# Performance work log

Measured on AMD Instinct MI355X. Metric: run time of the kernel, lower is better.

Reference implementation:

```python
import jax, jax.numpy as jnp
import numpy as np

B, H, S, D = 2, 16, 2048, 64  # depth = dmodel / num_heads
DMODEL = H * D


def setup_inputs() -> dict:
    key = jax.random.key(0)
    kq, kk, kv, kw = jax.random.split(key, 4)
    Q = jax.random.normal(kq, (B, H, S, D), dtype=jnp.float32)
    K = jax.random.normal(kk, (B, H, S, D), dtype=jnp.float32)
    V = jax.random.normal(kv, (B, H, S, D), dtype=jnp.float32)
    W = jax.random.normal(kw, (DMODEL, DMODEL), dtype=jnp.float32) * (1.0 / np.sqrt(DMODEL))
    b = jnp.zeros((DMODEL,), dtype=jnp.float32)
    return {"Q": Q, "K": K, "V": V, "W": W, "b": b}


def reference(Q, K, V, W, b):
    depth = Q.shape[-1]
    # scores: (B, H, S, S) -- full score matrix, matching the original math
    scores = jnp.einsum('bhqd,bhkd->bhqk', Q, K) / jnp.sqrt(jnp.float32(depth))
    attn = jax.nn.softmax(scores, axis=-1)
    vals = jnp.einsum('bhqk,bhkd->bhqd', attn, V)          # (B, H, S, D)
    vals = jnp.transpose(vals, (0, 2, 1, 3))               # (B, S, H, D)
    concat = vals.reshape(vals.shape[0], vals.shape[1], -1)  # (B, S, dmodel)
    return concat @ W + b
```

## Files before the change

### kernel.cpp

```cpp
#include <hip/hip_runtime.h>
#include <hip/hip_bf16.h>


typedef float  f32x16 __attribute__((ext_vector_type(16)));
typedef float  f32x4v __attribute__((ext_vector_type(4)));
typedef float  f32x2v __attribute__((ext_vector_type(2)));
typedef __bf16 bf16x8 __attribute__((ext_vector_type(8)));
typedef __bf16 bf16x4 __attribute__((ext_vector_type(4)));
typedef __bf16 bf16x2 __attribute__((ext_vector_type(2)));

static constexpr int Bn = 2, Hn = 16, Sn = 2048, Dn = 64, DM = 1024;
static constexpr size_t QKV_ELEMS = (size_t)Bn * Hn * Sn * Dn;

#define QSCALE 0.18033688011112042f

#define LGKM_BARRIER() do {                                  \
    asm volatile("s_waitcnt lgkmcnt(0)" ::: "memory");       \
    __builtin_amdgcn_s_barrier();                            \
  } while (0)

#if __has_builtin(__builtin_amdgcn_cvt_pk_bf16_f32)
static __device__ __forceinline__ unsigned pack2(float a, float b) {
  bf16x2 t = __builtin_amdgcn_cvt_pk_bf16_f32(a, b);
  union { bf16x2 v; unsigned u; } c; c.v = t; return c.u;
}
#else
static __device__ __forceinline__ unsigned pack2(float a, float b) {
  union { __bf16 h; unsigned short s; } ua, ub;
  ua.h = (__bf16)a; ub.h = (__bf16)b;
  return (unsigned)ua.s | ((unsigned)ub.s << 16);
}
#endif

static __device__ __forceinline__ void unzip8(const unsigned* wds, bf16x8* r0, bf16x8* r1) {
  union { unsigned u[4]; bf16x8 v; } a, b;
#pragma unroll
  for (int i = 0; i < 4; ++i) {
    unsigned lo = wds[2 * i], hi = wds[2 * i + 1];
    a.u[i] = (lo & 0xffffu) | (hi << 16);
    b.u[i] = (lo >> 16) | (hi & 0xffff0000u);
  }
  *r0 = a.v; *r1 = b.v;
}

__global__ __launch_bounds__(256) void convert_all(
    const float* __restrict__ k,
    const float* __restrict__ v, const float* __restrict__ w,
    __bf16* __restrict__ ko,
    __bf16* __restrict__ vt, __bf16* __restrict__ wt) {
  __shared__ __bf16 T[64][74];
  const int bid = blockIdx.x, t = threadIdx.x;

  if (bid < 2048) {
    size_t i = ((size_t)bid * 256 + t) * 8;
    f32x4v a = *(const f32x4v*)(k + i);
    f32x4v b = *(const f32x4v*)(k + i + 4);
    bf16x8 o;
#pragma unroll
    for (int j = 0; j < 4; ++j) { o[j] = (__bf16)a[j]; o[4 + j] = (__bf16)b[j]; }
    *(bf16x8*)(ko + i) = o;
    return;
  }

  const float* s0;
  __bf16* dst0;
  size_t dst_stride;
  {
    const int r = t >> 2, c0 = (t & 3) * 16;
    if (bid < 3072) {
      const int idx = bid - 2048;
      const int kv0 = (idx & 31) * 64, bh = idx >> 5;
      s0 = v + ((size_t)bh * Sn + kv0 + r) * Dn + c0;
      dst0 = vt + (size_t)bh * Dn * Sn + kv0;
      dst_stride = Sn;
    } else {
      const int idx = bid - 3072;
      const int nt = (idx & 15) * 64, kt = (idx >> 4) * 64;
      s0 = w + (size_t)(kt + r) * DM + nt + c0;
      dst0 = wt + (size_t)nt * DM + kt;
      dst_stride = DM;
    }
    union { bf16x8 v8; unsigned u[4]; } o0, o1;
#pragma unroll
    for (int i = 0; i < 2; ++i) {
      f32x4v f = *(const f32x4v*)(s0 + i * 4);
#pragma unroll
      for (int j = 0; j < 4; ++j) o0.v8[i * 4 + j] = (__bf16)f[j];
    }
#pragma unroll
    for (int i = 0; i < 2; ++i) {
      f32x4v f = *(const f32x4v*)(s0 + 8 + i * 4);
#pragma unroll
      for (int j = 0; j < 4; ++j) o1.v8[i * 4 + j] = (__bf16)f[j];
    }
#pragma unroll
    for (int j = 0; j < 4; ++j) {
      *(unsigned*)&T[r][c0 + 2 * j]     = o0.u[j];
      *(unsigned*)&T[r][c0 + 8 + 2 * j] = o1.u[j];
    }
  }
  __syncthreads();
  const int rp = t >> 3, k0 = (t & 7) * 8;
  unsigned wds[8];
#pragma unroll
  for (int i = 0; i < 8; ++i) wds[i] = *(const unsigned*)&T[k0 + i][2 * rp];
  bf16x8 r0, r1; unzip8(wds, &r0, &r1);
  __bf16* d0 = dst0 + (size_t)(2 * rp) * dst_stride + k0;
  *(bf16x8*)d0 = r0;
  *(bf16x8*)(d0 + dst_stride) = r1;
}

__global__ __launch_bounds__(512, 4) void attn(
    const float* __restrict__ Qf, const __bf16* __restrict__ Kb,
    const __bf16* __restrict__ Vtg, __bf16* __restrict__ Cc) {
  const int tid = threadIdx.x;
  const int wave = tid >> 6, lane = tid & 63;
  const int ln = lane & 31, g = lane >> 5;
  const int qg = wave >> 1, kh = wave & 1;
  const int qb = blockIdx.x, h = blockIdx.y, bz = blockIdx.z;

  __shared__ __bf16 Ks[2][128][72];
  __shared__ __bf16 Vs[2][64][136];

  const size_t hoff = (size_t)(bz * Hn + h) * Sn * Dn;
  const float*  Qp = Qf + hoff + (size_t)(qb * 128 + qg * 32) * Dn;
  const __bf16* Kp = Kb + hoff;
  const __bf16* Vp = Vtg + hoff;

  bf16x8 qf[4];
#pragma unroll
  for (int ks = 0; ks < 4; ++ks) {
    const float* qp = Qp + (size_t)ln * Dn + ks * 16 + g * 8;
    f32x4v f0 = *(const f32x4v*)qp;
    f32x4v f1 = *(const f32x4v*)(qp + 4);
#pragma unroll
    for (int j = 0; j < 4; ++j) {
      qf[ks][j]     = (__bf16)(f0[j] * QSCALE);
      qf[ks][4 + j] = (__bf16)(f1[j] * QSCALE);
    }
  }

  const int kr = tid >> 2, kc = (tid & 3) * 16;
  const int vr = tid >> 3, vc = (tid & 7) * 16;
  const __bf16* kbase = Kp + (size_t)kr * Dn + kc;
  const __bf16* vbase = Vp + (size_t)vr * Sn + vc;

  bf16x8 k0r = *(const bf16x8*)kbase, k1r = *(const bf16x8*)(kbase + 8);
  bf16x8 v0r = *(const bf16x8*)vbase, v1r = *(const bf16x8*)(vbase + 8);
  {
    *(bf16x8*)&Ks[0][kr][kc]     = k0r;
    *(bf16x8*)&Ks[0][kr][kc + 8] = k1r;
    union { bf16x8 v; bf16x4 h[2]; } u0, u1; u0.v = v0r; u1.v = v1r;
    union { bf16x4 h[2]; bf16x8 v; } w0, w1;
    w0.h[0] = u0.h[0]; w0.h[1] = u1.h[0];
    w1.h[0] = u0.h[1]; w1.h[1] = u1.h[1];
    *(bf16x8*)&Vs[0][vr][vc]     = w0.v;
    *(bf16x8*)&Vs[0][vr][vc + 8] = w1.v;
  }
  k0r = *(const bf16x8*)(kbase + (size_t)128 * Dn);
  k1r = *(const bf16x8*)(kbase + (size_t)128 * Dn + 8);
  v0r = *(const bf16x8*)(vbase + 128);
  v1r = *(const bf16x8*)(vbase + 128 + 8);
  LGKM_BARRIER();

  f32x16 O0 = {}, O1 = {};
  float Lown = 0.0f;
  constexpr int NT = Sn / 128;

  for (int kt = 0; kt < NT; ++kt) {
    const int buf = kt & 1;

    unsigned w[16];
#pragma unroll
    for (int m = 0; m < 2; ++m) {
      bf16x8 kf[4];
#pragma unroll
      for (int ks = 0; ks < 4; ++ks)
        kf[ks] = *(const bf16x8*)&Ks[buf][kh * 64 + m * 32 + ln][ks * 16 + g * 8];

      f32x16 s = {};
      __builtin_amdgcn_s_setprio(1);
#pragma unroll
      for (int ks = 0; ks < 4; ++ks)
        s = __builtin_amdgcn_mfma_f32_32x32x16_bf16(kf[ks], qf[ks], s, 0, 0, 0);
      __builtin_amdgcn_s_setprio(0);

      float p[16];
#pragma unroll
      for (int r = 0; r < 16; ++r) p[r] = __builtin_amdgcn_exp2f(s[r]);
      f32x2v s2 = {0.0f, 0.0f};
#pragma unroll
      for (int tt = 0; tt < 8; ++tt) { f32x2v t2 = {p[2 * tt], p[2 * tt + 1]}; s2 += t2; }
      Lown += s2[0] + s2[1];
#pragma unroll
      for (int tt = 0; tt < 8; ++tt) w[m * 8 + tt] = pack2(p[2 * tt], p[2 * tt + 1]);
    }

    if (kt + 1 < NT) {
      const int nb = buf ^ 1;
      *(bf16x8*)&Ks[nb][kr][kc]     = k0r;
      *(bf16x8*)&Ks[nb][kr][kc + 8] = k1r;
      union { bf16x8 v; bf16x4 h[2]; } u0, u1; u0.v = v0r; u1.v = v1r;
      union { bf16x4 h[2]; bf16x8 v; } w0, w1;
      w0.h[0] = u0.h[0]; w0.h[1] = u1.h[0];
      w1.h[0] = u0.h[1]; w1.h[1] = u1.h[1];
      *(bf16x8*)&Vs[nb][vr][vc]     = w0.v;
      *(bf16x8*)&Vs[nb][vr][vc + 8] = w1.v;
      if (kt + 2 < NT) {
        const __bf16* kp = kbase + (size_t)(kt + 2) * 128 * Dn;
        k0r = *(const bf16x8*)kp; k1r = *(const bf16x8*)(kp + 8);
        const __bf16* vp = vbase + (kt + 2) * 128;
        v0r = *(const bf16x8*)vp; v1r = *(const bf16x8*)(vp + 8);
      }
    }

    __builtin_amdgcn_s_setprio(1);
#pragma unroll
    for (int s4 = 0; s4 < 4; ++s4) {
      const int cb = kh * 64 + s4 * 16 + g * 8;
      bf16x8 vf0 = *(const bf16x8*)&Vs[buf][ln][cb];
      bf16x8 vf1 = *(const bf16x8*)&Vs[buf][32 + ln][cb];
      union { unsigned u[4]; bf16x8 v; } pu;
      pu.u[0] = w[s4 * 4 + 0];
      pu.u[1] = w[s4 * 4 + 1];
      pu.u[2] = w[s4 * 4 + 2];
      pu.u[3] = w[s4 * 4 + 3];
      O0 = __builtin_amdgcn_mfma_f32_32x32x16_bf16(vf0, pu.v, O0, 0, 0, 0);
      O1 = __builtin_amdgcn_mfma_f32_32x32x16_bf16(vf1, pu.v, O1, 0, 0, 0);
    }
    __builtin_amdgcn_s_setprio(0);

    LGKM_BARRIER();
  }

  const float Lred = Lown + __shfl_xor(Lown, 32);
  float* Ex = (float*)Ks;
  const int slot = (qg * 64 + lane) * 36;
  if (kh == 1) {
#pragma unroll
    for (int i = 0; i < 4; ++i) {
      f32x4v t = {O0[4 * i], O0[4 * i + 1], O0[4 * i + 2], O0[4 * i + 3]};
      *(f32x4v*)&Ex[slot + 4 * i] = t;
    }
#pragma unroll
    for (int i = 0; i < 4; ++i) {
      f32x4v t = {O1[4 * i], O1[4 * i + 1], O1[4 * i + 2], O1[4 * i + 3]};
      *(f32x4v*)&Ex[slot + 16 + 4 * i] = t;
    }
    Ex[slot + 32] = Lred;
  }
  __syncthreads();
  __bf16* T = (__bf16*)Vs;
  if (kh == 0) {
    float inv;
#pragma unroll
    for (int i = 0; i < 4; ++i) {
      f32x4v t = *(const f32x4v*)&Ex[slot + 4 * i];
#pragma unroll
      for (int c = 0; c < 4; ++c) O0[4 * i + c] += t[c];
    }
#pragma unroll
    for (int i = 0; i < 4; ++i) {
      f32x4v t = *(const f32x4v*)&Ex[slot + 16 + 4 * i];
#pragma unroll
      for (int c = 0; c < 4; ++c) O1[4 * i + c] += t[c];
    }
    inv = 1.0f / (Lred + Ex[slot + 32]);
#pragma unroll
    for (int dh = 0; dh < 2; ++dh) {
#pragma unroll
      for (int a = 0; a < 4; ++a) {
        const f32x16 O = dh ? O1 : O0;
        bf16x4 t4;
#pragma unroll
        for (int c = 0; c < 4; ++c) t4[c] = (__bf16)(O[4 * a + c] * inv);
        *(bf16x4*)&T[(qg * 32 + ln) * 72 + dh * 32 + 8 * a + 4 * g] = t4;
      }
    }
  }
  __syncthreads();
  const int q0 = qb * 128;
#pragma unroll
  for (int i = 0; i < 2; ++i) {
    const int rq = i * 64 + (tid >> 3);
    const int c8 = (tid & 7) * 8;
    bf16x8 o = *(const bf16x8*)&T[rq * 72 + c8];
    size_t base = (((size_t)bz * Sn + q0 + rq) * Hn + h) * Dn + c8;
    *(bf16x8*)&Cc[base] = o;
  }
}

__global__ __launch_bounds__(512, 2) void proj(
    const __bf16* __restrict__ A, const __bf16* __restrict__ Wt,
    const float* __restrict__ bias, float* __restrict__ out) {
  const int tid = threadIdx.x, wave = tid >> 6, lane = tid & 63;
  const int ln = lane & 31, g = lane >> 5;
  const int mq = wave >> 1, nh = wave & 1;
  const int bm = blockIdx.x, bn = blockIdx.y;
  __shared__ __bf16 As[2][128][72];
  __shared__ __bf16 Bs[2][64][72];
  const int ar = tid >> 2, ac = (tid & 3) * 16;
  const int rb = tid >> 3, cb = (tid & 7) * 8;
  f32x16 acc = {};
  const __bf16* Ap = A + (size_t)(bm * 128) * DM;
  const __bf16* Wp = Wt + (size_t)(bn * 64) * DM;

  bf16x8 a0, a1, b0;
  {
    const __bf16* ap = Ap + (size_t)ar * DM + ac;
    a0 = *(const bf16x8*)ap; a1 = *(const bf16x8*)(ap + 8);
    b0 = *(const bf16x8*)(Wp + (size_t)rb * DM + cb);
  }
  *(bf16x8*)&As[0][ar][ac]     = a0;
  *(bf16x8*)&As[0][ar][ac + 8] = a1;
  *(bf16x8*)&Bs[0][rb][cb]     = b0;
  {
    const __bf16* ap = Ap + (size_t)ar * DM + 64 + ac;
    a0 = *(const bf16x8*)ap; a1 = *(const bf16x8*)(ap + 8);
    b0 = *(const bf16x8*)(Wp + (size_t)rb * DM + 64 + cb);
  }
  LGKM_BARRIER();

  constexpr int KT = DM / 64;
  for (int kt = 0; kt < KT; ++kt) {
    const int buf = kt & 1;
    __builtin_amdgcn_s_setprio(1);
#pragma unroll
    for (int ks = 0; ks < 4; ++ks) {
      bf16x8 af = *(const bf16x8*)&As[buf][mq * 32 + ln][ks * 16 + g * 8];
      bf16x8 wf = *(const bf16x8*)&Bs[buf][nh * 32 + ln][ks * 16 + g * 8];
      acc = __builtin_amdgcn_mfma_f32_32x32x16_bf16(af, wf, acc, 0, 0, 0);
    }
    __builtin_amdgcn_s_setprio(0);
    if (kt + 1 < KT) {
      const int nb = buf ^ 1;
      *(bf16x8*)&As[nb][ar][ac]     = a0;
      *(bf16x8*)&As[nb][ar][ac + 8] = a1;
      *(bf16x8*)&Bs[nb][rb][cb]     = b0;
      if (kt + 2 < KT) {
        const __bf16* ap = Ap + (size_t)ar * DM + (kt + 2) * 64 + ac;
        a0 = *(const bf16x8*)ap; a1 = *(const bf16x8*)(ap + 8);
        b0 = *(const bf16x8*)(Wp + (size_t)rb * DM + (kt + 2) * 64 + cb);
      }
    }
    LGKM_BARRIER();
  }
  const float bv = bias[bn * 64 + nh * 32 + ln];
#pragma unroll
  for (int r = 0; r < 16; ++r) {
    int row = bm * 128 + mq * 32 + (r & 3) + 8 * (r >> 2) + 4 * g;
    out[(size_t)row * DM + bn * 64 + nh * 32 + ln] = acc[r] + bv;
  }
}

extern "C" void kernel_launch(void* const* d_in, const int* in_sizes, int n_in,
                              void* d_out, int out_size, void* d_ws, size_t ws_size,
                              hipStream_t stream) {
  const float* Q = (const float*)d_in[0];
  const float* K = (const float*)d_in[1];
  const float* V = (const float*)d_in[2];
  const float* W = (const float*)d_in[3];
  const float* b = (const float*)d_in[4];
  float* out = (float*)d_out;

  __bf16* ws  = (__bf16*)d_ws;
  __bf16* Kb  = ws;
  __bf16* Vtg = Kb + QKV_ELEMS;
  __bf16* Cc  = Vtg + QKV_ELEMS;
  __bf16* Wt  = Cc + QKV_ELEMS;

  convert_all<<<dim3(3328, 1, 1), 256, 0, stream>>>(K, V, W, Kb, Vtg, Wt);
  attn<<<dim3(Sn / 128, Hn, Bn), 512, 0, stream>>>(Q, Kb, Vtg, Cc);
  proj<<<dim3(Bn * Sn / 128, DM / 64, 1), 512, 0, stream>>>(Cc, Wt, b, out);
}
```

Measured before the change: 157.5 us.

## Split attention blocks into 64 queries with four-way key split and single LDS buffer

The attention kernel now processes 64 queries per block instead of 128, doubling the grid to 1024 blocks. Each pair of query waves splits every 128-key tile four ways instead of two, and the partial outputs are merged with a two-stage LDS tree reduction. The K/V staging drops from double-buffered to a single buffer, with an extra barrier placed before the next tile is written. The flat grid also uses a block-index swizzle to spread heads across the XCDs. This gives more blocks and less LDS per block, in exchange for more redundant K/V loads per query, extra barriers each iteration, and a longer reduction at the end.

```diff
diff --git a/kernel.cpp b/kernel.cpp
--- a/kernel.cpp
+++ b/kernel.cpp
@@ -113,17 +113,20 @@
 __global__ __launch_bounds__(512, 4) void attn(
     const float* __restrict__ Qf, const __bf16* __restrict__ Kb,
     const __bf16* __restrict__ Vtg, __bf16* __restrict__ Cc) {
+  __shared__ __align__(16) unsigned char lds_raw[36864];
+  __bf16 (*Ks)[72]  = (__bf16 (*)[72])lds_raw;
+  __bf16 (*Vs)[136] = (__bf16 (*)[136])(lds_raw + 18432);
+
   const int tid = threadIdx.x;
   const int wave = tid >> 6, lane = tid & 63;
   const int ln = lane & 31, g = lane >> 5;
-  const int qg = wave >> 1, kh = wave & 1;
-  const int qb = blockIdx.x, h = blockIdx.y, bz = blockIdx.z;
-
-  __shared__ __bf16 Ks[2][128][72];
-  __shared__ __bf16 Vs[2][64][136];
+  const int qg = wave >> 2, kh = wave & 3;
+  const int f = blockIdx.x;
+  const int swz = (f & 7) * 128 + (f >> 3);
+  const int qb = swz & 31, h = (swz >> 5) & 15, bz = swz >> 9;
 
   const size_t hoff = (size_t)(bz * Hn + h) * Sn * Dn;
-  const float*  Qp = Qf + hoff + (size_t)(qb * 128 + qg * 32) * Dn;
+  const float*  Qp = Qf + hoff + (size_t)(qb * 64 + qg * 32) * Dn;
   const __bf16* Kp = Kb + hoff;
   const __bf16* Vp = Vtg + hoff;
 
@@ -148,14 +151,14 @@
   bf16x8 k0r = *(const bf16x8*)kbase, k1r = *(const bf16x8*)(kbase + 8);
   bf16x8 v0r = *(const bf16x8*)vbase, v1r = *(const bf16x8*)(vbase + 8);
   {
-    *(bf16x8*)&Ks[0][kr][kc]     = k0r;
-    *(bf16x8*)&Ks[0][kr][kc + 8] = k1r;
+    *(bf16x8*)&Ks[kr][kc]     = k0r;
+    *(bf16x8*)&Ks[kr][kc + 8] = k1r;
     union { bf16x8 v; bf16x4 h[2]; } u0, u1; u0.v = v0r; u1.v = v1r;
     union { bf16x4 h[2]; bf16x8 v; } w0, w1;
     w0.h[0] = u0.h[0]; w0.h[1] = u1.h[0];
     w1.h[0] = u0.h[1]; w1.h[1] = u1.h[1];
-    *(bf16x8*)&Vs[0][vr][vc]     = w0.v;
-    *(bf16x8*)&Vs[0][vr][vc + 8] = w1.v;
+    *(bf16x8*)&Vs[vr][vc]     = w0.v;
+    *(bf16x8*)&Vs[vr][vc + 8] = w1.v;
   }
   k0r = *(const bf16x8*)(kbase + (size_t)128 * Dn);
   k1r = *(const bf16x8*)(kbase + (size_t)128 * Dn + 8);
@@ -168,44 +171,33 @@
   constexpr int NT = Sn / 128;
 
   for (int kt = 0; kt < NT; ++kt) {
-    const int buf = kt & 1;
-
-    unsigned w[16];
-#pragma unroll
-    for (int m = 0; m < 2; ++m) {
-      bf16x8 kf[4];
-#pragma unroll
-      for (int ks = 0; ks < 4; ++ks)
-        kf[ks] = *(const bf16x8*)&Ks[buf][kh * 64 + m * 32 + ln][ks * 16 + g * 8];
-
-      f32x16 s = {};
-      __builtin_amdgcn_s_setprio(1);
-#pragma unroll
-      for (int ks = 0; ks < 4; ++ks)
-        s = __builtin_amdgcn_mfma_f32_32x32x16_bf16(kf[ks], qf[ks], s, 0, 0, 0);
-      __builtin_amdgcn_s_setprio(0);
-
-      float p[16];
-#pragma unroll
-      for (int r = 0; r < 16; ++r) p[r] = __builtin_amdgcn_exp2f(s[r]);
-      f32x2v s2 = {0.0f, 0.0f};
-#pragma unroll
-      for (int tt = 0; tt < 8; ++tt) { f32x2v t2 = {p[2 * tt], p[2 * tt + 1]}; s2 += t2; }
-      Lown += s2[0] + s2[1];
-#pragma unroll
-      for (int tt = 0; tt < 8; ++tt) w[m * 8 + tt] = pack2(p[2 * tt], p[2 * tt + 1]);
-    }
+    bf16x8 kf[4];
+#pragma unroll
+    for (int ks = 0; ks < 4; ++ks)
+      kf[ks] = *(const bf16x8*)&Ks[kh * 32 + ln][ks * 16 + g * 8];
+
+    f32x16 s = {};
+#pragma unroll
+    for (int ks = 0; ks < 4; ++ks)
+      s = __builtin_amdgcn_mfma_f32_32x32x16_bf16(kf[ks], qf[ks], s, 0, 0, 0);
+
+    const int cb = kh * 32 + g * 8;
+    bf16x8 vf00 = *(const bf16x8*)&Vs[ln][cb];
+    bf16x8 vf01 = *(const bf16x8*)&Vs[32 + ln][cb];
+    bf16x8 vf10 = *(const bf16x8*)&Vs[ln][cb + 16];
+    bf16x8 vf11 = *(const bf16x8*)&Vs[32 + ln][cb + 16];
+
+    LGKM_BARRIER();
 
     if (kt + 1 < NT) {
-      const int nb = buf ^ 1;
-      *(bf16x8*)&Ks[nb][kr][kc]     = k0r;
-      *(bf16x8*)&Ks[nb][kr][kc + 8] = k1r;
+      *(bf16x8*)&Ks[kr][kc]     = k0r;
+      *(bf16x8*)&Ks[kr][kc + 8] = k1r;
       union { bf16x8 v; bf16x4 h[2]; } u0, u1; u0.v = v0r; u1.v = v1r;
       union { bf16x4 h[2]; bf16x8 v; } w0, w1;
       w0.h[0] = u0.h[0]; w0.h[1] = u1.h[0];
       w1.h[0] = u0.h[1]; w1.h[1] = u1.h[1];
-      *(bf16x8*)&Vs[nb][vr][vc]     = w0.v;
-      *(bf16x8*)&Vs[nb][vr][vc + 8] = w1.v;
+      *(bf16x8*)&Vs[vr][vc]     = w0.v;
+      *(bf16x8*)&Vs[vr][vc + 8] = w1.v;
       if (kt + 2 < NT) {
         const __bf16* kp = kbase + (size_t)(kt + 2) * 128 * Dn;
         k0r = *(const bf16x8*)kp; k1r = *(const bf16x8*)(kp + 8);
@@ -214,58 +206,102 @@
       }
     }
 
-    __builtin_amdgcn_s_setprio(1);
-#pragma unroll
-    for (int s4 = 0; s4 < 4; ++s4) {
-      const int cb = kh * 64 + s4 * 16 + g * 8;
-      bf16x8 vf0 = *(const bf16x8*)&Vs[buf][ln][cb];
-      bf16x8 vf1 = *(const bf16x8*)&Vs[buf][32 + ln][cb];
+    float p[16];
+#pragma unroll
+    for (int r = 0; r < 16; ++r) p[r] = __builtin_amdgcn_exp2f(s[r]);
+    f32x2v s2 = {0.0f, 0.0f};
+#pragma unroll
+    for (int tt = 0; tt < 8; ++tt) { f32x2v t2 = {p[2 * tt], p[2 * tt + 1]}; s2 += t2; }
+    Lown += s2[0] + s2[1];
+    unsigned w[8];
+#pragma unroll
+    for (int tt = 0; tt < 8; ++tt) w[tt] = pack2(p[2 * tt], p[2 * tt + 1]);
+
+#pragma unroll
+    for (int s4 = 0; s4 < 2; ++s4) {
       union { unsigned u[4]; bf16x8 v; } pu;
       pu.u[0] = w[s4 * 4 + 0];
       pu.u[1] = w[s4 * 4 + 1];
       pu.u[2] = w[s4 * 4 + 2];
       pu.u[3] = w[s4 * 4 + 3];
-      O0 = __builtin_amdgcn_mfma_f32_32x32x16_bf16(vf0, pu.v, O0, 0, 0, 0);
-      O1 = __builtin_amdgcn_mfma_f32_32x32x16_bf16(vf1, pu.v, O1, 0, 0, 0);
-    }
-    __builtin_amdgcn_s_setprio(0);
+      O0 = __builtin_amdgcn_mfma_f32_32x32x16_bf16(s4 ? vf10 : vf00, pu.v, O0, 0, 0, 0);
+      O1 = __builtin_amdgcn_mfma_f32_32x32x16_bf16(s4 ? vf11 : vf01, pu.v, O1, 0, 0, 0);
+    }
 
     LGKM_BARRIER();
   }
 
-  const float Lred = Lown + __shfl_xor(Lown, 32);
-  float* Ex = (float*)Ks;
-  const int slot = (qg * 64 + lane) * 36;
-  if (kh == 1) {
-#pragma unroll
-    for (int i = 0; i < 4; ++i) {
-      f32x4v t = {O0[4 * i], O0[4 * i + 1], O0[4 * i + 2], O0[4 * i + 3]};
-      *(f32x4v*)&Ex[slot + 4 * i] = t;
-    }
-#pragma unroll
-    for (int i = 0; i < 4; ++i) {
-      f32x4v t = {O1[4 * i], O1[4 * i + 1], O1[4 * i + 2], O1[4 * i + 3]};
-      *(f32x4v*)&Ex[slot + 16 + 4 * i] = t;
-    }
-    Ex[slot + 32] = Lred;
-  }
-  __syncthreads();
-  __bf16* T = (__bf16*)Vs;
+  float Lacc = Lown + __shfl_xor(Lown, 32);
+  float* Ex = (float*)lds_raw;
+  {
+    const int slot = (((qg << 1) | (kh >> 1)) * 64 + lane) * 36;
+    if (kh & 1) {
+#pragma unroll
+      for (int i = 0; i < 4; ++i) {
+        f32x4v t = {O0[4 * i], O0[4 * i + 1], O0[4 * i + 2], O0[4 * i + 3]};
+        *(f32x4v*)&Ex[slot + 4 * i] = t;
+      }
+#pragma unroll
+      for (int i = 0; i < 4; ++i) {
+        f32x4v t = {O1[4 * i], O1[4 * i + 1], O1[4 * i + 2], O1[4 * i + 3]};
+        *(f32x4v*)&Ex[slot + 16 + 4 * i] = t;
+      }
+      Ex[slot + 32] = Lacc;
+    }
+    __syncthreads();
+    if (!(kh & 1)) {
+#pragma unroll
+      for (int i = 0; i < 4; ++i) {
+        f32x4v t = *(const f32x4v*)&Ex[slot + 4 * i];
+#pragma unroll
+        for (int c = 0; c < 4; ++c) O0[4 * i + c] += t[c];
+      }
+#pragma unroll
+      for (int i = 0; i < 4; ++i) {
+        f32x4v t = *(const f32x4v*)&Ex[slot + 16 + 4 * i];
+#pragma unroll
+        for (int c = 0; c < 4; ++c) O1[4 * i + c] += t[c];
+      }
+      Lacc += Ex[slot + 32];
+    }
+    __syncthreads();
+  }
+  float inv = 0.0f;
+  {
+    const int slot2 = (qg * 64 + lane) * 36;
+    if (kh == 2) {
+#pragma unroll
+      for (int i = 0; i < 4; ++i) {
+        f32x4v t = {O0[4 * i], O0[4 * i + 1], O0[4 * i + 2], O0[4 * i + 3]};
+        *(f32x4v*)&Ex[slot2 + 4 * i] = t;
+      }
+#pragma unroll
+      for (int i = 0; i < 4; ++i) {
+        f32x4v t = {O1[4 * i], O1[4 * i + 1], O1[4 * i + 2], O1[4 * i + 3]};
+        *(f32x4v*)&Ex[slot2 + 16 + 4 * i] = t;
+      }
+      Ex[slot2 + 32] = Lacc;
+    }
+    __syncthreads();
+    if (kh == 0) {
+#pragma unroll
+      for (int i = 0; i < 4; ++i) {
+        f32x4v t = *(const f32x4v*)&Ex[slot2 + 4 * i];
+#pragma unroll
+        for (int c = 0; c < 4; ++c) O0[4 * i + c] += t[c];
+      }
+#pragma unroll
+      for (int i = 0; i < 4; ++i) {
+        f32x4v t = *(const f32x4v*)&Ex[slot2 + 16 + 4 * i];
+#pragma unroll
+        for (int c = 0; c < 4; ++c) O1[4 * i + c] += t[c];
+      }
+      inv = 1.0f / (Lacc + Ex[slot2 + 32]);
+    }
+    __syncthreads();
+  }
+  __bf16* T = (__bf16*)lds_raw;
   if (kh == 0) {
-    float inv;
-#pragma unroll
-    for (int i = 0; i < 4; ++i) {
-      f32x4v t = *(const f32x4v*)&Ex[slot + 4 * i];
-#pragma unroll
-      for (int c = 0; c < 4; ++c) O0[4 * i + c] += t[c];
-    }
-#pragma unroll
-    for (int i = 0; i < 4; ++i) {
-      f32x4v t = *(const f32x4v*)&Ex[slot + 16 + 4 * i];
-#pragma unroll
-      for (int c = 0; c < 4; ++c) O1[4 * i + c] += t[c];
-    }
-    inv = 1.0f / (Lred + Ex[slot + 32]);
 #pragma unroll
     for (int dh = 0; dh < 2; ++dh) {
 #pragma unroll
@@ -279,10 +315,9 @@
     }
   }
   __syncthreads();
-  const int q0 = qb * 128;
-#pragma unroll
-  for (int i = 0; i < 2; ++i) {
-    const int rq = i * 64 + (tid >> 3);
+  const int q0 = qb * 64;
+  {
+    const int rq = tid >> 3;
     const int c8 = (tid & 7) * 8;
     bf16x8 o = *(const bf16x8*)&T[rq * 72 + c8];
     size_t base = (((size_t)bz * Sn + q0 + rq) * Hn + h) * Dn + c8;
@@ -370,6 +405,6 @@
   __bf16* Wt  = Cc + QKV_ELEMS;
 
   convert_all<<<dim3(3328, 1, 1), 256, 0, stream>>>(K, V, W, Kb, Vtg, Wt);
-  attn<<<dim3(Sn / 128, Hn, Bn), 512, 0, stream>>>(Q, Kb, Vtg, Cc);
+  attn<<<dim3(1024, 1, 1), 512, 0, stream>>>(Q, Kb, Vtg, Cc);
   proj<<<dim3(Bn * Sn / 128, DM / 64, 1), 512, 0, stream>>>(Cc, Wt, b, out);
 }
```

After: 166.1 us. +5.5%, slower.
